# Kernel optimization log

Measured on AMD Instinct MI355X. Metric: run time of the kernel, lower is better.

The kernel has to match this reference:

```python
import jax, jax.numpy as jnp
import numpy as np

B, K, T, C = 4, 8, 2048, 64

def setup_inputs() -> dict:
    key = jax.random.key(0)
    ks = jax.random.split(key, 7)
    return {
        "x": jax.random.normal(ks[0], (B, K, T, C), dtype=jnp.float32),
        "Wq": jax.random.normal(ks[1], (C, C), dtype=jnp.float32) / np.sqrt(C),
        "bq": jax.random.normal(ks[2], (C,), dtype=jnp.float32) * 0.01,
        "Wk": jax.random.normal(ks[3], (C, C), dtype=jnp.float32) / np.sqrt(C),
        "bk": jax.random.normal(ks[4], (C,), dtype=jnp.float32) * 0.01,
        "Wv": jax.random.normal(ks[5], (C, C), dtype=jnp.float32) / np.sqrt(C),
        "bv": jax.random.normal(ks[6], (C,), dtype=jnp.float32) * 0.01,
    }

def reference(x, Wq, bq, Wk, bk, Wv, bv):
    c_dim = x.shape[-1]
    # torch nn.Linear: y = x @ W.T + b
    q = jnp.einsum('bktc,dc->bktd', x, Wq) + bq
    k = jnp.einsum('bktc,dc->bktd', x, Wk) + bk
    v = jnp.einsum('bktc,dc->bktd', x, Wv) + bv
    scores = jnp.einsum('bkic,bkjc->bkij', q, k) / jnp.sqrt(jnp.float32(c_dim))
    attn = jax.nn.softmax(scores, axis=-1)
    out = jnp.einsum('bkij,bkjc->bkic', attn, v)
    return out
```

## Files before the change

kernel.cpp:

```cpp
#include <hip/hip_runtime.h>


#define T_DIM 2048
#define NHEAD 32
#define HSTRIDE (T_DIM * 64)
#define QSCALE 0.18033688011112042f
#define SOFF  8.0f

#define SWZ(row, grp) ((row) * 64 + ((((grp) ^ ((row) & 7)) & 7) * 8))

typedef _Float16 h8 __attribute__((ext_vector_type(8)));
typedef _Float16 h4 __attribute__((ext_vector_type(4)));
typedef __fp16   g2 __attribute__((ext_vector_type(2)));
typedef float    f4 __attribute__((ext_vector_type(4)));
typedef float    fv16 __attribute__((ext_vector_type(16)));

union H4U { h4 v; g2 p[2]; };
union H8U { h8 v; h4 h[2]; g2 p[4]; };

#if defined(__has_builtin)
#if __has_builtin(__builtin_amdgcn_exp2f)
#define EXP2(x) __builtin_amdgcn_exp2f(x)
#endif
#endif
#ifndef EXP2
__device__ inline float exp2_raw(float x) {
    float r;
    asm("v_exp_f32 %0, %1" : "=v"(r) : "v"(x));
    return r;
}
#define EXP2(x) exp2_raw(x)
#endif

__device__ inline h4 cvt4(f4 x) {
    H4U u;
    u.p[0] = __builtin_amdgcn_cvt_pkrtz(x[0], x[1]);
    u.p[1] = __builtin_amdgcn_cvt_pkrtz(x[2], x[3]);
    return u.v;
}

__device__ inline h8 cvt8(f4 a, f4 b) {
    H8U r;
    r.h[0] = cvt4(a);
    r.h[1] = cvt4(b);
    return r.v;
}

__device__ inline fv16 splat16(float x) {
    fv16 r;
    #pragma unroll
    for (int i = 0; i < 16; ++i) r[i] = x;
    return r;
}

__global__ __launch_bounds__(256) void qkv_proj_kernel(
    const float* __restrict__ x,
    const float* __restrict__ Wq, const float* __restrict__ bq,
    const float* __restrict__ Wk, const float* __restrict__ bk,
    const float* __restrict__ Wv, const float* __restrict__ bv,
    _Float16* __restrict__ qh, _Float16* __restrict__ khT,
    _Float16* __restrict__ vtT)
{
    __shared__ _Float16 ws[3][64 * 64];
    __shared__ float bsh[3][64];

    const int tid  = threadIdx.x;
    const int row0 = blockIdx.x * 64;
    const int head = blockIdx.x >> 5;
    const int t0   = (blockIdx.x & 31) * 64;

    const int w    = tid >> 6;
    const int lane = tid & 63;
    const int l15  = lane & 15;
    const int qd   = lane >> 4;

    f4 xa[2][2];
    {
        const float* xp = x + (size_t)(row0 + w * 16 + l15) * 64 + qd * 8;
        #pragma unroll
        for (int ch = 0; ch < 2; ++ch) {
            xa[ch][0] = *(const f4*)(xp + ch * 32);
            xa[ch][1] = *(const f4*)(xp + ch * 32 + 4);
        }
    }

    #pragma unroll
    for (int m = 0; m < 3; ++m) {
        const float* Wm = (m == 0) ? Wq : ((m == 1) ? Wk : Wv);
        const float* bm = (m == 0) ? bq : ((m == 1) ? bk : bv);
        #pragma unroll
        for (int pass = 0; pass < 4; ++pass) {
            const int idx = pass * 1024 + tid * 4;
            const int d = idx >> 6, c = idx & 63;
            f4 wv = *(const f4*)(Wm + idx);
            *(h4*)&ws[m][SWZ(d, c >> 3) + (c & 7)] = cvt4(wv);
        }
        if (tid < 64) bsh[m][tid] = bm[tid];
    }

    h8 af[2];
    #pragma unroll
    for (int ch = 0; ch < 2; ++ch)
        af[ch] = cvt8(xa[ch][0], xa[ch][1]);

    __syncthreads();

    f4 acc[3][4];
    #pragma unroll
    for (int m = 0; m < 3; ++m) {
        h8 bf[4][2];
        #pragma unroll
        for (int ns = 0; ns < 4; ++ns)
            #pragma unroll
            for (int ch = 0; ch < 2; ++ch)
                bf[ns][ch] = *(const h8*)&ws[m][SWZ(ns * 16 + l15, ch * 4 + qd)];
        #pragma unroll
        for (int ns = 0; ns < 4; ++ns)
            acc[m][ns] = (f4){0.f, 0.f, 0.f, 0.f};
        #pragma unroll
        for (int ch = 0; ch < 2; ++ch)
            #pragma unroll
            for (int ns = 0; ns < 4; ++ns)
                acc[m][ns] = __builtin_amdgcn_mfma_f32_16x16x32_f16(
                    af[ch], bf[ns][ch], acc[m][ns], 0, 0, 0);
    }

    __syncthreads();

    #pragma unroll
    for (int m = 0; m < 2; ++m) {
        #pragma unroll
        for (int ns = 0; ns < 4; ++ns) {
            const int d = ns * 16 + l15;
            const float bias = bsh[m][d];
            #pragma unroll
            for (int r = 0; r < 4; ++r) {
                const int t = w * 16 + qd * 4 + r;
                float v = acc[m][ns][r] + bias;
                if (m == 0) v *= QSCALE;
                ws[m][SWZ(t, d >> 3) + (d & 7)] = (_Float16)v;
            }
        }
    }
    #pragma unroll
    for (int ns = 0; ns < 4; ++ns) {
        const int d = ns * 16 + l15;
        const float bias = bsh[2][d];
        const int tl = w * 16 + qd * 4;
        f4 pvf;
        #pragma unroll
        for (int r = 0; r < 4; ++r)
            pvf[r] = acc[2][ns][r] + bias;
        *(h4*)&ws[2][SWZ(d, tl >> 3) + (tl & 7)] = cvt4(pvf);
    }

    __syncthreads();

    #pragma unroll
    for (int pass = 0; pass < 2; ++pass) {
        const int t  = pass * 32 + (tid >> 3);
        const int c0 = (tid & 7) * 8;
        *(h8*)&qh[(size_t)(row0 + t) * 64 + c0] =
            *(const h8*)&ws[0][SWZ(t, tid & 7)];
    }
    #pragma unroll
    for (int pass = 0; pass < 2; ++pass) {
        const int f   = pass * 2048 + tid * 8;
        const int kb  = f >> 11;
        const int cs  = (f >> 9) & 3;
        const int l   = (f >> 3) & 63;
        const int p   = l & 31;
        const int w16 = p & 15;
        const int sw  = ((w16 & 12) == 4) ? (w16 + 4)
                      : (((w16 & 12) == 8) ? (w16 - 4) : w16);
        const int tact = kb * 32 + (p & 16) + sw;
        const int g8   = cs * 2 + (l >> 5);
        *(h8*)&khT[(size_t)head * HSTRIDE + (t0 >> 6) * 4096 + f] =
            *(const h8*)&ws[1][SWZ(tact, g8)];
    }
    #pragma unroll
    for (int pass = 0; pass < 2; ++pass) {
        const int f  = pass * 2048 + tid * 8;
        const int q2 = f >> 9;
        const int b  = q2 >> 1, cc = q2 & 1;
        const int l  = (f >> 3) & 63;
        const int c  = cc * 32 + (l & 31);
        const int tg = b * 2 + (l >> 5);
        *(h8*)&vtT[(size_t)head * HSTRIDE + (t0 >> 6) * 4096 + f] =
            *(const h8*)&ws[2][SWZ(c, tg)];
    }
}

__global__ __launch_bounds__(256, 2) void attn_kernel(
    const _Float16* __restrict__ qh, const _Float16* __restrict__ khT,
    const _Float16* __restrict__ vtT, float* __restrict__ out)
{
    __shared__ float xbuf[4][2304];

    const int tid  = threadIdx.x;
    const int w    = tid >> 6;
    const int lane = tid & 63;
    const int l31  = lane & 31;
    const int lh   = lane >> 5;
    const int qg   = w >> 1;
    const int ph   = w & 1;

    const int bid  = blockIdx.x;
    const int xcd  = bid & 7;
    const int slot = bid >> 3;
    const int head = xcd * 4 + (slot >> 4);
    const int qpart = slot & 15;
    const int q0   = qpart * 128 + qg * 64;

    h8 qf[2][4];
    #pragma unroll
    for (int qs = 0; qs < 2; ++qs) {
        const _Float16* qp = qh + (size_t)(head * T_DIM + q0 + qs * 32 + l31) * 64 + lh * 8;
        #pragma unroll
        for (int cs = 0; cs < 4; ++cs)
            qf[qs][cs] = *(const h8*)(qp + cs * 16);
    }

    const int ko = lane * 8;
    const _Float16* kbase = khT + (size_t)head * HSTRIDE + (size_t)ph * 16 * 4096;
    const _Float16* vbase = vtT + (size_t)head * HSTRIDE + (size_t)ph * 16 * 4096;

    f4 rs4[2] = {(f4){0.f,0.f,0.f,0.f}, (f4){0.f,0.f,0.f,0.f}};
    fv16 oacc[2][2];
    #pragma unroll
    for (int qs = 0; qs < 2; ++qs)
        #pragma unroll
        for (int cc = 0; cc < 2; ++cc)
            oacc[qs][cc] = splat16(0.f);

    h8 kf[2][4];
    h8 vf[4][2];
    #pragma unroll
    for (int kb = 0; kb < 2; ++kb)
        #pragma unroll
        for (int cs = 0; cs < 4; ++cs)
            kf[kb][cs] = *(const h8*)(kbase + kb * 2048 + cs * 512 + ko);
    #pragma unroll
    for (int b = 0; b < 4; ++b)
        #pragma unroll
        for (int cc = 0; cc < 2; ++cc)
            vf[b][cc] = *(const h8*)(vbase + (b * 2 + cc) * 512 + ko);

    for (int it = 0; it < 16; ++it) {
        const _Float16* kn = kbase + (size_t)(it + 1) * 4096;
        const _Float16* vn = vbase + (size_t)(it + 1) * 4096;
        const bool more = (it < 15);

        #pragma unroll
        for (int kb = 0; kb < 2; ++kb) {
            fv16 st2[2];
            st2[0] = splat16(-SOFF);
            st2[1] = splat16(-SOFF);
            #pragma unroll
            for (int cs = 0; cs < 4; ++cs)
                #pragma unroll
                for (int qs = 0; qs < 2; ++qs)
                    st2[qs] = __builtin_amdgcn_mfma_f32_32x32x16_f16(
                        kf[kb][cs], qf[qs][cs], st2[qs], 0, 0, 0);

            if (more) {
                #pragma unroll
                for (int cs = 0; cs < 4; ++cs)
                    kf[kb][cs] = *(const h8*)(kn + kb * 2048 + cs * 512 + ko);
            }

            #pragma unroll
            for (int qs = 0; qs < 2; ++qs) {
                f4 pg[4];
                #pragma unroll
                for (int g = 0; g < 4; ++g) {
                    pg[g][0] = EXP2(st2[qs][4 * g + 0]);
                    pg[g][1] = EXP2(st2[qs][4 * g + 1]);
                    pg[g][2] = EXP2(st2[qs][4 * g + 2]);
                    pg[g][3] = EXP2(st2[qs][4 * g + 3]);
                    rs4[qs] += pg[g];
                }
                H8U pa[2];
                #pragma unroll
                for (int g = 0; g < 4; ++g) {
                    pa[g >> 1].p[(g & 1) * 2 + 0] = __builtin_amdgcn_cvt_pkrtz(pg[g][0], pg[g][1]);
                    pa[g >> 1].p[(g & 1) * 2 + 1] = __builtin_amdgcn_cvt_pkrtz(pg[g][2], pg[g][3]);
                }
                #pragma unroll
                for (int bl = 0; bl < 2; ++bl)
                    #pragma unroll
                    for (int cc = 0; cc < 2; ++cc)
                        oacc[qs][cc] = __builtin_amdgcn_mfma_f32_32x32x16_f16(
                            pa[bl].v, vf[kb * 2 + bl][cc], oacc[qs][cc], 0, 0, 0);
            }

            if (more) {
                #pragma unroll
                for (int bl = 0; bl < 2; ++bl)
                    #pragma unroll
                    for (int cc = 0; cc < 2; ++cc)
                        vf[kb * 2 + bl][cc] =
                            *(const h8*)(vn + ((kb * 2 + bl) * 2 + cc) * 512 + ko);
            }
        }
    }

    const int wqs = ph ^ 1;
    {
        float* xb = xbuf[w];
        #pragma unroll
        for (int cc = 0; cc < 2; ++cc)
            #pragma unroll
            for (int r = 0; r < 16; ++r)
                xb[(cc * 16 + r) * 64 + lane] = oacc[wqs][cc][r];
        #pragma unroll
        for (int i = 0; i < 4; ++i)
            xb[2048 + i * 64 + lane] = rs4[wqs][i];
    }

    __syncthreads();

    const float* pb = xbuf[w ^ 1];
    const int f = ph;
    fv16 of[2];
    #pragma unroll
    for (int cc = 0; cc < 2; ++cc)
        #pragma unroll
        for (int r = 0; r < 16; ++r)
            of[cc][r] = oacc[f][cc][r] + pb[(cc * 16 + r) * 64 + lane];
    f4 rsf;
    #pragma unroll
    for (int i = 0; i < 4; ++i)
        rsf[i] = rs4[f][i] + pb[2048 + i * 64 + lane];

    float lsum = (rsf[0] + rsf[1]) + (rsf[2] + rsf[3]);
    lsum += __shfl_xor(lsum, 32, 64);
    const float linv = 1.f / lsum;
    #pragma unroll
    for (int r = 0; r < 16; ++r) {
        const int qrow = (r & 3) + 8 * (r >> 2) + 4 * lh;
        const float fac = __shfl(linv, qrow, 64);
        #pragma unroll
        for (int cc = 0; cc < 2; ++cc)
            out[(size_t)(head * T_DIM + q0 + f * 32 + qrow) * 64 + cc * 32 + l31] =
                of[cc][r] * fac;
    }
}

extern "C" void kernel_launch(void* const* d_in, const int* in_sizes, int n_in,
                              void* d_out, int out_size, void* d_ws, size_t ws_size,
                              hipStream_t stream)
{
    (void)in_sizes; (void)n_in; (void)out_size; (void)ws_size;
    const float* x  = (const float*)d_in[0];
    const float* Wq = (const float*)d_in[1];
    const float* bq = (const float*)d_in[2];
    const float* Wk = (const float*)d_in[3];
    const float* bk = (const float*)d_in[4];
    const float* Wv = (const float*)d_in[5];
    const float* bv = (const float*)d_in[6];
    float* out = (float*)d_out;

    _Float16* qh  = (_Float16*)d_ws;
    _Float16* khT = qh + (size_t)NHEAD * HSTRIDE;
    _Float16* vtT = khT + (size_t)NHEAD * HSTRIDE;

    hipLaunchKernelGGL(qkv_proj_kernel, dim3(1024), dim3(256), 0, stream,
                       x, Wq, bq, Wk, bk, Wv, bv, qh, khT, vtT);
    hipLaunchKernelGGL(attn_kernel, dim3(512), dim3(256), 0, stream,
                       qh, khT, vtT, out);
}
```

Measured before the change: 134.1 us.

## Give each wave its own 32 query rows over the full key range

Work in the attention kernel is now split by query rows only. Previously two waves split the key range and each covered 64 query rows, then merged partial output and row sums through shared memory. Now each wave handles 32 query rows across all 32 key iterations, so the LDS buffer, the barrier and the final reduction disappear and fewer registers hold accumulators. In exchange, each loaded K/V fragment feeds only one QK MFMA instead of two, so global/L2 traffic per FLOP doubles and each wave's serial loop runs twice as long.

Measured after the change: 126.3 us. 5.9% less time.

```diff
diff --git a/kernel.cpp b/kernel.cpp
--- a/kernel.cpp
+++ b/kernel.cpp
@@ -195,43 +195,35 @@
     const _Float16* __restrict__ qh, const _Float16* __restrict__ khT,
     const _Float16* __restrict__ vtT, float* __restrict__ out)
 {
-    __shared__ float xbuf[4][2304];
-
     const int tid  = threadIdx.x;
     const int w    = tid >> 6;
     const int lane = tid & 63;
     const int l31  = lane & 31;
     const int lh   = lane >> 5;
-    const int qg   = w >> 1;
-    const int ph   = w & 1;
 
     const int bid  = blockIdx.x;
     const int xcd  = bid & 7;
     const int slot = bid >> 3;
     const int head = xcd * 4 + (slot >> 4);
     const int qpart = slot & 15;
-    const int q0   = qpart * 128 + qg * 64;
-
-    h8 qf[2][4];
-    #pragma unroll
-    for (int qs = 0; qs < 2; ++qs) {
-        const _Float16* qp = qh + (size_t)(head * T_DIM + q0 + qs * 32 + l31) * 64 + lh * 8;
+    const int q0w  = qpart * 128 + w * 32;
+
+    h8 qf[4];
+    {
+        const _Float16* qp = qh + (size_t)(head * T_DIM + q0w + l31) * 64 + lh * 8;
         #pragma unroll
         for (int cs = 0; cs < 4; ++cs)
-            qf[qs][cs] = *(const h8*)(qp + cs * 16);
+            qf[cs] = *(const h8*)(qp + cs * 16);
     }
 
     const int ko = lane * 8;
-    const _Float16* kbase = khT + (size_t)head * HSTRIDE + (size_t)ph * 16 * 4096;
-    const _Float16* vbase = vtT + (size_t)head * HSTRIDE + (size_t)ph * 16 * 4096;
-
-    f4 rs4[2] = {(f4){0.f,0.f,0.f,0.f}, (f4){0.f,0.f,0.f,0.f}};
-    fv16 oacc[2][2];
-    #pragma unroll
-    for (int qs = 0; qs < 2; ++qs)
-        #pragma unroll
-        for (int cc = 0; cc < 2; ++cc)
-            oacc[qs][cc] = splat16(0.f);
+    const _Float16* kbase = khT + (size_t)head * HSTRIDE;
+    const _Float16* vbase = vtT + (size_t)head * HSTRIDE;
+
+    f4 rs4 = (f4){0.f, 0.f, 0.f, 0.f};
+    fv16 oacc[2];
+    oacc[0] = splat16(0.f);
+    oacc[1] = splat16(0.f);
 
     h8 kf[2][4];
     h8 vf[4][2];
@@ -246,22 +238,18 @@
         for (int cc = 0; cc < 2; ++cc)
             vf[b][cc] = *(const h8*)(vbase + (b * 2 + cc) * 512 + ko);
 
-    for (int it = 0; it < 16; ++it) {
+    for (int it = 0; it < 32; ++it) {
         const _Float16* kn = kbase + (size_t)(it + 1) * 4096;
         const _Float16* vn = vbase + (size_t)(it + 1) * 4096;
-        const bool more = (it < 15);
+        const bool more = (it < 31);
 
         #pragma unroll
         for (int kb = 0; kb < 2; ++kb) {
-            fv16 st2[2];
-            st2[0] = splat16(-SOFF);
-            st2[1] = splat16(-SOFF);
+            fv16 st = splat16(-SOFF);
             #pragma unroll
             for (int cs = 0; cs < 4; ++cs)
-                #pragma unroll
-                for (int qs = 0; qs < 2; ++qs)
-                    st2[qs] = __builtin_amdgcn_mfma_f32_32x32x16_f16(
-                        kf[kb][cs], qf[qs][cs], st2[qs], 0, 0, 0);
+                st = __builtin_amdgcn_mfma_f32_32x32x16_f16(
+                    kf[kb][cs], qf[cs], st, 0, 0, 0);
 
             if (more) {
                 #pragma unroll
@@ -269,30 +257,27 @@
                     kf[kb][cs] = *(const h8*)(kn + kb * 2048 + cs * 512 + ko);
             }
 
-            #pragma unroll
-            for (int qs = 0; qs < 2; ++qs) {
-                f4 pg[4];
+            f4 pg[4];
+            #pragma unroll
+            for (int g = 0; g < 4; ++g) {
+                pg[g][0] = EXP2(st[4 * g + 0]);
+                pg[g][1] = EXP2(st[4 * g + 1]);
+                pg[g][2] = EXP2(st[4 * g + 2]);
+                pg[g][3] = EXP2(st[4 * g + 3]);
+                rs4 += pg[g];
+            }
+            H8U pa[2];
+            #pragma unroll
+            for (int g = 0; g < 4; ++g) {
+                pa[g >> 1].p[(g & 1) * 2 + 0] = __builtin_amdgcn_cvt_pkrtz(pg[g][0], pg[g][1]);
+                pa[g >> 1].p[(g & 1) * 2 + 1] = __builtin_amdgcn_cvt_pkrtz(pg[g][2], pg[g][3]);
+            }
+            #pragma unroll
+            for (int bl = 0; bl < 2; ++bl)
                 #pragma unroll
-                for (int g = 0; g < 4; ++g) {
-                    pg[g][0] = EXP2(st2[qs][4 * g + 0]);
-                    pg[g][1] = EXP2(st2[qs][4 * g + 1]);
-                    pg[g][2] = EXP2(st2[qs][4 * g + 2]);
-                    pg[g][3] = EXP2(st2[qs][4 * g + 3]);
-                    rs4[qs] += pg[g];
-                }
-                H8U pa[2];
-                #pragma unroll
-                for (int g = 0; g < 4; ++g) {
-                    pa[g >> 1].p[(g & 1) * 2 + 0] = __builtin_amdgcn_cvt_pkrtz(pg[g][0], pg[g][1]);
-                    pa[g >> 1].p[(g & 1) * 2 + 1] = __builtin_amdgcn_cvt_pkrtz(pg[g][2], pg[g][3]);
-                }
-                #pragma unroll
-                for (int bl = 0; bl < 2; ++bl)
-                    #pragma unroll
-                    for (int cc = 0; cc < 2; ++cc)
-                        oacc[qs][cc] = __builtin_amdgcn_mfma_f32_32x32x16_f16(
-                            pa[bl].v, vf[kb * 2 + bl][cc], oacc[qs][cc], 0, 0, 0);
-            }
+                for (int cc = 0; cc < 2; ++cc)
+                    oacc[cc] = __builtin_amdgcn_mfma_f32_32x32x16_f16(
+                        pa[bl].v, vf[kb * 2 + bl][cc], oacc[cc], 0, 0, 0);
 
             if (more) {
                 #pragma unroll
@@ -305,35 +290,7 @@
         }
     }
 
-    const int wqs = ph ^ 1;
-    {
-        float* xb = xbuf[w];
-        #pragma unroll
-        for (int cc = 0; cc < 2; ++cc)
-            #pragma unroll
-            for (int r = 0; r < 16; ++r)
-                xb[(cc * 16 + r) * 64 + lane] = oacc[wqs][cc][r];
-        #pragma unroll
-        for (int i = 0; i < 4; ++i)
-            xb[2048 + i * 64 + lane] = rs4[wqs][i];
-    }
-
-    __syncthreads();
-
-    const float* pb = xbuf[w ^ 1];
-    const int f = ph;
-    fv16 of[2];
-    #pragma unroll
-    for (int cc = 0; cc < 2; ++cc)
-        #pragma unroll
-        for (int r = 0; r < 16; ++r)
-            of[cc][r] = oacc[f][cc][r] + pb[(cc * 16 + r) * 64 + lane];
-    f4 rsf;
-    #pragma unroll
-    for (int i = 0; i < 4; ++i)
-        rsf[i] = rs4[f][i] + pb[2048 + i * 64 + lane];
-
-    float lsum = (rsf[0] + rsf[1]) + (rsf[2] + rsf[3]);
+    float lsum = (rs4[0] + rs4[1]) + (rs4[2] + rs4[3]);
     lsum += __shfl_xor(lsum, 32, 64);
     const float linv = 1.f / lsum;
     #pragma unroll
@@ -342,8 +299,8 @@
         const float fac = __shfl(linv, qrow, 64);
         #pragma unroll
         for (int cc = 0; cc < 2; ++cc)
-            out[(size_t)(head * T_DIM + q0 + f * 32 + qrow) * 64 + cc * 32 + l31] =
-                of[cc][r] * fac;
+            out[(size_t)(head * T_DIM + q0w + qrow) * 64 + cc * 32 + l31] =
+                oacc[cc][r] * fac;
     }
 }
 
```
